# Performance work log

Measured on AMD Instinct MI355X. Metric: run time of the kernel, lower is better.

Reference implementation:

```python
import jax, jax.numpy as jnp
import numpy as np

B, CIN, COUT, K, STRIDE, PAD = 32, 64, 128, 3, 1, 1
IN_H, IN_W = 112, 112


def setup_inputs() -> dict:
    key = jax.random.key(0)
    k1, k2 = jax.random.split(key)
    # x_padded already has `PAD` rows/cols of zeros on each side, as in the torch module
    x = jax.random.normal(k1, (B, CIN, IN_H, IN_W), dtype=jnp.float32)
    x_padded = jnp.pad(x, ((0, 0), (0, 0), (PAD, PAD), (PAD, PAD)))
    weight = jax.random.normal(k2, (COUT, CIN, K, K), dtype=jnp.float32) * 0.1
    bias = jnp.zeros((COUT,), dtype=jnp.float32)
    return {
        "x_padded": x_padded,
        "in_height": IN_H,
        "in_width": IN_W,
        "weight": weight,
        "bias": bias,
    }


def reference(x_padded, in_height, in_width, weight, bias):
    # CustomConv2D.custom_conv2d: direct conv over the pre-padded input.
    # out[b,o,h,w] = sum_{i,kh,kw} x_padded[b,i,h*s+kh,w*s+kw] * weight[o,i,kh,kw] + bias[o]
    out = jax.lax.conv_general_dilated(
        x_padded, weight,
        window_strides=(STRIDE, STRIDE),
        padding="VALID",  # padding already applied to x_padded
        dimension_numbers=("NCHW", "OIHW", "NCHW"),
    )
    return out + bias[None, :, None, None]
```

## Files before the change

kernel.cpp:

```cpp
#include <hip/hip_runtime.h>

typedef __attribute__((ext_vector_type(8))) short short8;
typedef __attribute__((ext_vector_type(4))) float f32x4;
typedef __attribute__((ext_vector_type(4))) unsigned int u32x4;
typedef unsigned short u16;
typedef unsigned int u32;

#define XH 114
#define XW 114
#define CINC 64
#define COUT 128
#define OH 112
#define OW 112
#define NB 32
#define KTOT 576
#define TILEB 58368

static __device__ __forceinline__ u16 f2bf(float f) {
    u32 x = __float_as_uint(f);
    u32 r = (x + 0x7fffu + ((x >> 16) & 1u)) >> 16;
    return (u16)r;
}

#define MFMA16(a, b, c) __builtin_amdgcn_mfma_f32_16x16x32_bf16((a), (b), (c), 0, 0, 0)

static __device__ __forceinline__ void gload16(const void* g, void* l) {
    __builtin_amdgcn_global_load_lds(
        (const __attribute__((address_space(1))) unsigned int*)g,
        (__attribute__((address_space(3))) unsigned int*)l, 16, 0, 0);
}


__global__ __launch_bounds__(256) void prep(const float* __restrict__ x,
                                            const float* __restrict__ w,
                                            u16* __restrict__ xb,
                                            u16* __restrict__ wbf) {
    const int tid = threadIdx.x;
    const int blk = blockIdx.x;
    if (blk >= NB * XH) {
        int i = (blk - NB * XH) * 256 + tid;
        int o = i / KTOT;
        int rem = i - o * KTOT;
        int khkw = rem >> 6;
        int ci = rem & 63;
        wbf[i] = f2bf(w[(o * CINC + ci) * 9 + khkw]);
        return;
    }
    __shared__ u16 tile[XW * 70];
    const int b = blk / XH;
    const int h = blk - b * XH;

    #pragma unroll
    for (int it = 0; it < 15; ++it) {
        int idx = it * 256 + tid;
        if (idx < 32 * XW) {
            int cp = idx / XW;
            int w_ = idx - cp * XW;
            const float* s0 = x + ((size_t)(b * CINC + 2 * cp) * XH + h) * XW + w_;
            float a = s0[0];
            float c = s0[XH * XW];
            u32 pk = (u32)f2bf(a) | ((u32)f2bf(c) << 16);
            *(u32*)&tile[w_ * 70 + 2 * cp] = pk;
        }
    }
    __syncthreads();

    u16* dstrow = xb + (size_t)(b * XH + h) * (XW * CINC);
    #pragma unroll
    for (int p2 = 0; p2 < 4; ++p2) {
        int task = p2 * 256 + tid;
        if (task < XW * 8) {
            int w_ = task >> 3;
            int c8 = task & 7;
            const u32* s = (const u32*)&tile[w_ * 70 + c8 * 8];
            u32x4 v = {s[0], s[1], s[2], s[3]};
            int slot = c8 ^ ((2 * h + w_) & 7);
            *(u32x4*)(dstrow + w_ * CINC + slot * 8) = v;
        }
    }
}

__global__ __launch_bounds__(512, 2) void conv_pers2(const u16* __restrict__ xb,
                                                     const u16* __restrict__ wbf,
                                                     const float* __restrict__ bias,
                                                     float* __restrict__ out) {
    __shared__ u16 lds[2 * 4 * XW * CINC];
    char* ldsc = (char*)lds;

    const int tid  = threadIdx.x;
    const int lane = tid & 63;
    const int wv   = tid >> 6;
    const int l16  = lane & 15;
    const int lhi  = lane >> 4;
    const int wm   = wv & 3;
    const int wn   = wv >> 2;

    int bidx = blockIdx.x;
    { int xcd = bidx & 7; bidx = xcd * 32 + (bidx >> 3); }
    const int t0g = bidx * 7;

    const u16* wrow0 = wbf + (wm * 32 + l16) * KTOT + lhi * 8;
    const u16* wrow1 = wrow0 + 16 * KTOT;
    short8 areg[18][2];
    #pragma unroll
    for (int t = 0; t < 18; ++t) {
        areg[t][0] = *(const short8*)(wrow0 + t * 32);
        areg[t][1] = *(const short8*)(wrow1 + t * 32);
    }
    const float bv0 = bias[wm * 32 + l16];
    const float bv1 = bias[wm * 32 + 16 + l16];

    {
        const int tg = t0g;
        const char* src = (const char*)(xb + (size_t)((tg / 56) * XH + (tg % 56) * 2) * (XW * CINC));
        #pragma unroll
        for (int it = 0; it < 8; ++it) {
            int off = it * 8192 + wv * 1024;
            if (off < TILEB) gload16(src + off + lane * 16, ldsc + off);
        }
    }
    __syncthreads();

    const f32x4 zero = {0.f, 0.f, 0.f, 0.f};

    #pragma unroll 1
    for (int i = 0; i < 7; ++i) {
        if (i < 6) {
            const int tg = t0g + i + 1;
            const char* src = (const char*)(xb + (size_t)((tg / 56) * XH + (tg % 56) * 2) * (XW * CINC));
            char* dstb = ldsc + ((i + 1) & 1) * TILEB;
            #pragma unroll
            for (int it = 0; it < 8; ++it) {
                int off = it * 8192 + wv * 1024;
                if (off < TILEB) gload16(src + off + lane * 16, dstb + off);
            }
        }

        const int tg = t0g + i;
        const int bb  = tg / 56;
        const int hh0 = (tg - bb * 56) * 2;
        char* buf = ldsc + (i & 1) * TILEB;

        f32x4 acc[2][7];
        #pragma unroll
        for (int mf = 0; mf < 2; ++mf)
            #pragma unroll
            for (int nf = 0; nf < 7; ++nf) acc[mf][nf] = zero;

        #pragma unroll
        for (int tt = 0; tt < 9; ++tt) {
            const int kh = tt / 3;
            const int kw = tt - kh * 3;
            const int r  = wn + kh;
            const int pix0 = r * XW + kw + l16;
            const int hash = (2 * (hh0 + r) + kw + l16) & 7;
            const int ba0 = (pix0 << 7) + ((lhi ^ hash) << 4);

            __builtin_amdgcn_s_setprio(1);
            #pragma unroll
            for (int nf = 0; nf < 7; ++nf) {
                short8 bf = *(const short8*)(buf + ba0 + nf * 2048);
                acc[0][nf] = MFMA16(bf, areg[2 * tt][0], acc[0][nf]);
                acc[1][nf] = MFMA16(bf, areg[2 * tt][1], acc[1][nf]);
            }
            __builtin_amdgcn_s_setprio(0);

            __builtin_amdgcn_s_setprio(1);
            #pragma unroll
            for (int nf = 0; nf < 7; ++nf) {
                short8 bf = *(const short8*)(buf + (ba0 ^ 0x40) + nf * 2048);
                acc[0][nf] = MFMA16(bf, areg[2 * tt + 1][0], acc[0][nf]);
                acc[1][nf] = MFMA16(bf, areg[2 * tt + 1][1], acc[1][nf]);
            }
            __builtin_amdgcn_s_setprio(0);
        }

        #pragma unroll
        for (int mf = 0; mf < 2; ++mf) {
            const int o = wm * 32 + mf * 16 + l16;
            const float bv = mf ? bv1 : bv0;
            float* po = out + ((size_t)bb * COUT + o) * (OH * OW) + (hh0 + wn) * OW;
            #pragma unroll
            for (int nf = 0; nf < 7; ++nf) {
                f32x4 v = acc[mf][nf];
                v[0] += bv; v[1] += bv; v[2] += bv; v[3] += bv;
                *(f32x4*)(po + nf * 16 + lhi * 4) = v;
            }
        }

        __builtin_amdgcn_sched_barrier(0);
        asm volatile("s_waitcnt vmcnt(14) lgkmcnt(0)" ::: "memory");
        __builtin_amdgcn_sched_barrier(0);
        __builtin_amdgcn_s_barrier();
    }
}


#define BK 32
#define NSTEP 18
#define LDB 40

__global__ __launch_bounds__(256) void wcvt_ident(const float* __restrict__ w,
                                                  u16* __restrict__ wbf) {
    int i = blockIdx.x * 256 + threadIdx.x;
    if (i < COUT * KTOT) wbf[i] = f2bf(w[i]);
}

__global__ __launch_bounds__(256) void conv_fb(const float* __restrict__ x,
                                               const u16* __restrict__ wbf,
                                               const float* __restrict__ bias,
                                               float* __restrict__ out) {
    __shared__ u16 ldsB[OW * LDB];
    const int tid = threadIdx.x;
    int bid = blockIdx.x;
    { int xcd = bid & 7; bid = xcd * 448 + (bid >> 3); }
    const int b = bid / OH;
    const int h = bid - b * OH;
    const float* xbp = x + (size_t)b * (CINC * XH * XW);
    float* outb = out + (size_t)b * (COUT * OH * OW) + h * OW;
    const int lane = tid & 63, wv = tid >> 6, l16 = lane & 15, lhi = lane >> 4;
    const int m0 = wv * 32;
    const int sk = tid >> 3, sn0 = (tid & 7) * 14;
    f32x4 acc[2][7];
    const f32x4 zero = {0.f, 0.f, 0.f, 0.f};
    #pragma unroll
    for (int i = 0; i < 2; ++i)
        #pragma unroll
        for (int j = 0; j < 7; ++j) acc[i][j] = zero;
    for (int t = 0; t < NSTEP; ++t) {
        const int kg = t * BK + sk;
        const int ci = kg / 9;
        const int r9 = kg - ci * 9;
        const int kh = r9 / 3, kw = r9 - (r9 / 3) * 3;
        const float* src = xbp + ((size_t)ci * XH + (h + kh)) * XW + kw + sn0;
        __syncthreads();
        #pragma unroll
        for (int i = 0; i < 14; ++i) ldsB[(sn0 + i) * LDB + sk] = f2bf(src[i]);
        __syncthreads();
        short8 afrag[2];
        #pragma unroll
        for (int mf = 0; mf < 2; ++mf)
            afrag[mf] = *(const short8*)(wbf + (m0 + mf * 16 + l16) * KTOT + t * BK + lhi * 8);
        #pragma unroll
        for (int nf = 0; nf < 7; ++nf) {
            short8 bfrag = *(const short8*)&ldsB[(nf * 16 + l16) * LDB + lhi * 8];
            acc[0][nf] = MFMA16(afrag[0], bfrag, acc[0][nf]);
            acc[1][nf] = MFMA16(afrag[1], bfrag, acc[1][nf]);
        }
    }
    #pragma unroll
    for (int mf = 0; mf < 2; ++mf)
        #pragma unroll
        for (int j = 0; j < 4; ++j) {
            const int o = m0 + mf * 16 + lhi * 4 + j;
            const float bv = bias[o];
            #pragma unroll
            for (int nf = 0; nf < 7; ++nf)
                outb[(size_t)o * (OH * OW) + nf * 16 + l16] = acc[mf][nf][j] + bv;
        }
}

extern "C" void kernel_launch(void* const* d_in, const int* in_sizes, int n_in,
                              void* d_out, int out_size, void* d_ws, size_t ws_size,
                              hipStream_t stream) {
    const float* x    = (const float*)d_in[0];
    const float* w    = (const float*)d_in[3];
    const float* bias = (const float*)d_in[4];
    float* out = (float*)d_out;

    const size_t WBYTES = (size_t)COUT * KTOT * 2;
    const size_t XBYTES = (size_t)NB * XH * XW * CINC * 2;
    if (ws_size >= WBYTES + XBYTES) {
        u16* wbf = (u16*)d_ws;
        u16* xb  = (u16*)((char*)d_ws + WBYTES);
        prep<<<NB * XH + (COUT * KTOT) / 256, 256, 0, stream>>>(x, w, xb, wbf);
        conv_pers2<<<256, 512, 0, stream>>>(xb, wbf, bias, out);
    } else {
        u16* wbf = (u16*)d_ws;
        wcvt_ident<<<(COUT * KTOT + 255) / 256, 256, 0, stream>>>(w, wbf);
        conv_fb<<<NB * OH, 256, 0, stream>>>(x, wbf, bias, out);
    }
}
```

Baseline: 120.9 us.

## Replace double-buffered 4-row tiles with a 4-row LDS ring buffer

The persistent 512-thread kernel, which loaded a full 4-input-row tile for every pair of output rows, is replaced by a 256-thread kernel. Each block now owns 7 consecutive output rows of one image and keeps a 4-slot ring of input rows in LDS, staging just one new row per iteration. This removes the redundant reloading of overlapping halo rows, halves LDS use per block and launches twice as many blocks. Each wave now covers 32 output channels for one output row, and the s_setprio hints are dropped. In exchange, more loop iterations each carry their own barrier and synchronisation overhead.

```diff
diff --git a/kernel.cpp b/kernel.cpp
--- a/kernel.cpp
+++ b/kernel.cpp
@@ -14,7 +14,7 @@
 #define OW 112
 #define NB 32
 #define KTOT 576
-#define TILEB 58368
+#define ROWB 14592
 
 static __device__ __forceinline__ u16 f2bf(float f) {
     u32 x = __float_as_uint(f);
@@ -80,11 +80,11 @@
     }
 }
 
-__global__ __launch_bounds__(512, 2) void conv_pers2(const u16* __restrict__ xb,
-                                                     const u16* __restrict__ wbf,
-                                                     const float* __restrict__ bias,
-                                                     float* __restrict__ out) {
-    __shared__ u16 lds[2 * 4 * XW * CINC];
+__global__ __launch_bounds__(256, 2) void conv_ring(const u16* __restrict__ xb,
+                                                    const u16* __restrict__ wbf,
+                                                    const float* __restrict__ bias,
+                                                    float* __restrict__ out) {
+    __shared__ u16 lds[4 * XW * CINC];
     char* ldsc = (char*)lds;
 
     const int tid  = threadIdx.x;
@@ -92,54 +92,50 @@
     const int wv   = tid >> 6;
     const int l16  = lane & 15;
     const int lhi  = lane >> 4;
-    const int wm   = wv & 3;
-    const int wn   = wv >> 2;
 
     int bidx = blockIdx.x;
-    { int xcd = bidx & 7; bidx = xcd * 32 + (bidx >> 3); }
-    const int t0g = bidx * 7;
-
-    const u16* wrow0 = wbf + (wm * 32 + l16) * KTOT + lhi * 8;
+    { int xcd = bidx & 7; bidx = xcd * 64 + (bidx >> 3); }
+    const int bb = bidx >> 4;
+    const int h0 = (bidx & 15) * 7;
+
+    const u16* wrow0 = wbf + (wv * 32 + l16) * KTOT + lhi * 8;
     const u16* wrow1 = wrow0 + 16 * KTOT;
-    short8 areg[18][2];
+    short8 areg0[18], areg1[18];
     #pragma unroll
     for (int t = 0; t < 18; ++t) {
-        areg[t][0] = *(const short8*)(wrow0 + t * 32);
-        areg[t][1] = *(const short8*)(wrow1 + t * 32);
-    }
-    const float bv0 = bias[wm * 32 + l16];
-    const float bv1 = bias[wm * 32 + 16 + l16];
-
-    {
-        const int tg = t0g;
-        const char* src = (const char*)(xb + (size_t)((tg / 56) * XH + (tg % 56) * 2) * (XW * CINC));
-        #pragma unroll
-        for (int it = 0; it < 8; ++it) {
-            int off = it * 8192 + wv * 1024;
-            if (off < TILEB) gload16(src + off + lane * 16, ldsc + off);
-        }
-    }
-    __syncthreads();
+        areg0[t] = *(const short8*)(wrow0 + t * 32);
+        areg1[t] = *(const short8*)(wrow1 + t * 32);
+    }
+    const float bv0 = bias[wv * 32 + l16];
+    const float bv1 = bias[wv * 32 + 16 + l16];
+
+    auto STAGE = [&](int hin) {
+        const char* src = (const char*)(xb + (size_t)(bb * XH + hin) * (XW * CINC));
+        char* dst = ldsc + (hin & 3) * ROWB;
+        #pragma unroll
+        for (int it = 0; it < 4; ++it) {
+            const int c = it * 4 + wv;
+            const int off = c * 1024;
+            if (c < 14) {
+                gload16(src + off + lane * 16, dst + off);
+            } else if (c == 14) {
+                if (lane < 16) gload16(src + off + lane * 16, dst + off);
+            }
+        }
+    };
+
+    STAGE(h0); STAGE(h0 + 1); STAGE(h0 + 2);
+    __builtin_amdgcn_sched_barrier(0);
+    asm volatile("s_waitcnt vmcnt(0) lgkmcnt(0)" ::: "memory");
+    __builtin_amdgcn_sched_barrier(0);
+    __builtin_amdgcn_s_barrier();
 
     const f32x4 zero = {0.f, 0.f, 0.f, 0.f};
 
     #pragma unroll 1
     for (int i = 0; i < 7; ++i) {
-        if (i < 6) {
-            const int tg = t0g + i + 1;
-            const char* src = (const char*)(xb + (size_t)((tg / 56) * XH + (tg % 56) * 2) * (XW * CINC));
-            char* dstb = ldsc + ((i + 1) & 1) * TILEB;
-            #pragma unroll
-            for (int it = 0; it < 8; ++it) {
-                int off = it * 8192 + wv * 1024;
-                if (off < TILEB) gload16(src + off + lane * 16, dstb + off);
-            }
-        }
-
-        const int tg = t0g + i;
-        const int bb  = tg / 56;
-        const int hh0 = (tg - bb * 56) * 2;
-        char* buf = ldsc + (i & 1) * TILEB;
+        const int hrow = h0 + i;
+        if (i < 6) STAGE(hrow + 3);
 
         f32x4 acc[2][7];
         #pragma unroll
@@ -151,35 +147,30 @@
         for (int tt = 0; tt < 9; ++tt) {
             const int kh = tt / 3;
             const int kw = tt - kh * 3;
-            const int r  = wn + kh;
-            const int pix0 = r * XW + kw + l16;
-            const int hash = (2 * (hh0 + r) + kw + l16) & 7;
-            const int ba0 = (pix0 << 7) + ((lhi ^ hash) << 4);
-
-            __builtin_amdgcn_s_setprio(1);
+            const int hin = hrow + kh;
+            const int sb  = (hin & 3) * ROWB;
+            const int hash = (2 * hin + kw + l16) & 7;
+            const int ba0 = sb + ((kw + l16) << 7) + ((lhi ^ hash) << 4);
+
             #pragma unroll
             for (int nf = 0; nf < 7; ++nf) {
-                short8 bf = *(const short8*)(buf + ba0 + nf * 2048);
-                acc[0][nf] = MFMA16(bf, areg[2 * tt][0], acc[0][nf]);
-                acc[1][nf] = MFMA16(bf, areg[2 * tt][1], acc[1][nf]);
-            }
-            __builtin_amdgcn_s_setprio(0);
-
-            __builtin_amdgcn_s_setprio(1);
+                short8 bf = *(const short8*)(ldsc + ba0 + nf * 2048);
+                acc[0][nf] = MFMA16(bf, areg0[2 * tt], acc[0][nf]);
+                acc[1][nf] = MFMA16(bf, areg1[2 * tt], acc[1][nf]);
+            }
             #pragma unroll
             for (int nf = 0; nf < 7; ++nf) {
-                short8 bf = *(const short8*)(buf + (ba0 ^ 0x40) + nf * 2048);
-                acc[0][nf] = MFMA16(bf, areg[2 * tt + 1][0], acc[0][nf]);
-                acc[1][nf] = MFMA16(bf, areg[2 * tt + 1][1], acc[1][nf]);
-            }
-            __builtin_amdgcn_s_setprio(0);
+                short8 bf = *(const short8*)(ldsc + (ba0 ^ 0x40) + nf * 2048);
+                acc[0][nf] = MFMA16(bf, areg0[2 * tt + 1], acc[0][nf]);
+                acc[1][nf] = MFMA16(bf, areg1[2 * tt + 1], acc[1][nf]);
+            }
         }
 
         #pragma unroll
         for (int mf = 0; mf < 2; ++mf) {
-            const int o = wm * 32 + mf * 16 + l16;
+            const int o = wv * 32 + mf * 16 + l16;
             const float bv = mf ? bv1 : bv0;
-            float* po = out + ((size_t)bb * COUT + o) * (OH * OW) + (hh0 + wn) * OW;
+            float* po = out + ((size_t)bb * COUT + o) * (OH * OW) + hrow * OW;
             #pragma unroll
             for (int nf = 0; nf < 7; ++nf) {
                 f32x4 v = acc[mf][nf];
@@ -274,7 +265,7 @@
         u16* wbf = (u16*)d_ws;
         u16* xb  = (u16*)((char*)d_ws + WBYTES);
         prep<<<NB * XH + (COUT * KTOT) / 256, 256, 0, stream>>>(x, w, xb, wbf);
-        conv_pers2<<<256, 512, 0, stream>>>(xb, wbf, bias, out);
+        conv_ring<<<512, 256, 0, stream>>>(xb, wbf, bias, out);
     } else {
         u16* wbf = (u16*)d_ws;
         wcvt_ident<<<(COUT * KTOT + 255) / 256, 256, 0, stream>>>(w, wbf);
```

Result: faster. 110.5 us (-8.7%).
